# Kernel tuning notes

Hardware: AMD Instinct MI355X
Metric: run time of the kernel (lower is better)

Reference implementation:

```python
import jax, jax.numpy as jnp
import numpy as np

B, N, D = 16384, 20, 13  # batch of states, agents per state, per-agent joint-state dim
SELF_STATE = 6           # self_state_size in SARL


def setup_inputs() -> dict:
    key = jax.random.key(0)
    ks = jax.random.split(key, 16)

    def init(k, fi, fo):
        # haiku MLP default: truncated-normal-ish std 1/sqrt(fan_in), zero bias
        return jax.random.normal(k, (fi, fo), jnp.float32) / np.float32(np.sqrt(fi))

    z = lambda n: jnp.zeros((n,), jnp.float32)
    return {
        "x": jax.random.normal(ks[0], (B, N, D), jnp.float32),
        # mlp1: 13 -> 150 -> 100, relu, activate_final=True
        "w1a": init(ks[1], D, 150), "b1a": z(150),
        "w1b": init(ks[2], 150, 100), "b1b": z(100),
        # attention: 200 -> 100 -> 100 -> 1
        "wa0": init(ks[3], 200, 100), "ba0": z(100),
        "wa1": init(ks[4], 100, 100), "ba1": z(100),
        "wa2": init(ks[5], 100, 1), "ba2": z(1),
        # mlp2: 100 -> 100 -> 50
        "w2a": init(ks[6], 100, 100), "b2a": z(100),
        "w2b": init(ks[7], 100, 50), "b2b": z(50),
        # mlp3: 56 -> 150 -> 100 -> 100 -> 1
        "w3a": init(ks[8], SELF_STATE + 50, 150), "b3a": z(150),
        "w3b": init(ks[9], 150, 100), "b3b": z(100),
        "w3c": init(ks[10], 100, 100), "b3c": z(100),
        "w3d": init(ks[11], 100, 1), "b3d": z(1),
    }


def reference(x, w1a, b1a, w1b, b1b, wa0, ba0, wa1, ba1, wa2, ba2,
              w2a, b2a, w2b, b2b, w3a, b3a, w3b, b3b, w3c, b3c, w3d, b3d):
    relu = jax.nn.relu
    # mlp1 (activate_final=True): [B,N,100]
    h1 = relu(relu(x @ w1a + b1a) @ w1b + b1b)
    # mean-pool over agents -> global state, broadcast + concat: [B,N,200]
    g = jnp.mean(h1, axis=1, keepdims=True)
    att_in = jnp.concatenate([h1, jnp.broadcast_to(g, h1.shape)], axis=-1)
    # attention MLP -> scores [B,N], softmax over agents
    s = relu(att_in @ wa0 + ba0)
    s = relu(s @ wa1 + ba1)
    scores = (s @ wa2 + ba2)[..., 0]
    attn = jax.nn.softmax(scores, axis=-1)
    # mlp2 features [B,N,50], softmax-weighted sum over agents -> [B,50]
    f = relu(h1 @ w2a + b2a) @ w2b + b2b
    wf = jnp.einsum('bnf,bn->bf', f, attn)
    # concat self-state (first row's first 6 dims) with pooled features -> [B,56]
    self_state = x[:, 0, :SELF_STATE]
    m = jnp.concatenate([self_state, wf], axis=-1)
    # mlp3: 56 -> 150 -> 100 -> 100 -> 1
    h = relu(m @ w3a + b3a)
    h = relu(h @ w3b + b3b)
    h = relu(h @ w3c + b3c)
    return h @ w3d + b3d  # [B,1] state value
```

## Files before the change

### kernel.cpp

```cpp
#include <hip/hip_runtime.h>
#include <math.h>

#define NT     512
#define NWAVES 8
#define GB     4
#define NTOK   20
#define NTT_P  5

typedef _Float16 f16x8 __attribute__((ext_vector_type(8)));
typedef _Float16 f16x4 __attribute__((ext_vector_type(4)));
typedef _Float16 f16x2 __attribute__((ext_vector_type(2)));
typedef float    f32x4 __attribute__((ext_vector_type(4)));

#define PHASE_BAR() do {                                      \
    asm volatile("s_waitcnt lgkmcnt(0)" ::: "memory");        \
    __builtin_amdgcn_s_barrier();                             \
    asm volatile("" ::: "memory");                            \
    __builtin_amdgcn_sched_barrier(0);                        \
} while (0)

#define WS_W1A  0
#define WS_W1B  5120
#define WS_WA0  23040
#define WS_WA1  37376
#define WS_W2A  51712
#define WS_W2B  66048
#define WS_W3A  74240
#define WS_W3B  84480
#define WS_W3C  102400
#define WS_WA0H 116736
#define WS_TOTAL 131072
#define WB_BASE 65536
#define WB_B1A  0
#define WB_B1B  160
#define WB_BA0  272
#define WB_BA1  384
#define WB_B2A  496
#define WB_B2B  608
#define WB_B3A  672
#define WB_B3B  832
#define WB_B3C  944
#define WB_WA2  1056
#define WB_N    1168
#define PREP_TOTAL (WS_TOTAL + WB_N)
#define WS_MV   135168

#define LH_A    0
#define LH_B    12160
#define LH_C    23040
#define LH_T1   LH_A
#define LH_S1   LH_A
#define LH_F1   LH_A
#define LH_H1   LH_B
#define LH_FF   LH_B
#define LH_GQ   LH_C
#define LF_PART 11520
#define LF_GB   12672
#define LF_ATT  13120
#define LF_SS   13200
#define LDS_DW  13224
#define LDS_BYTES (LDS_DW * 4)

#define TB      64
#define TL_MV   0
#define TL_HA   4608
#define TL_HB   15360
#define TL_HC   24064
#define LDS_T_DW   16384
#define LDS_T_BYTES (LDS_T_DW * 4)

__device__ __forceinline__ void prep_one(const float* __restrict__ src, _Float16* dst,
                                         int local, int N, int K, int Ks)
{
    int n = local / Ks, k = local - n * Ks;
    dst[local] = (_Float16)((n < N && k < K) ? src[k * N + n] : 0.f);
}
__device__ __forceinline__ void prep_b(const float* __restrict__ src, float* dst,
                                       int idx, int N)
{
    dst[idx] = (idx < N) ? src[idx] : 0.f;
}

__global__ __launch_bounds__(256)
void prep_kernel(const float* __restrict__ w1a, const float* __restrict__ w1b,
                 const float* __restrict__ wa0, const float* __restrict__ wa1,
                 const float* __restrict__ w2a, const float* __restrict__ w2b,
                 const float* __restrict__ w3a, const float* __restrict__ w3b,
                 const float* __restrict__ w3c, const float* __restrict__ wa2,
                 const float* __restrict__ b1a, const float* __restrict__ b1b,
                 const float* __restrict__ ba0, const float* __restrict__ ba1,
                 const float* __restrict__ b2a, const float* __restrict__ b2b,
                 const float* __restrict__ b3a, const float* __restrict__ b3b,
                 const float* __restrict__ b3c,
                 _Float16* __restrict__ ws)
{
    int g = blockIdx.x * 256 + threadIdx.x;
    if (g >= PREP_TOTAL) return;
    if (g >= WS_TOTAL) {
        float* wb = (float*)ws + WB_BASE;
        int l = g - WS_TOTAL;
        if (l < WB_B1B)      prep_b(b1a, wb + WB_B1A, l - WB_B1A, 150);
        else if (l < WB_BA0) prep_b(b1b, wb + WB_B1B, l - WB_B1B, 100);
        else if (l < WB_BA1) prep_b(ba0, wb + WB_BA0, l - WB_BA0, 100);
        else if (l < WB_B2A) prep_b(ba1, wb + WB_BA1, l - WB_BA1, 100);
        else if (l < WB_B2B) prep_b(b2a, wb + WB_B2A, l - WB_B2A, 100);
        else if (l < WB_B3A) prep_b(b2b, wb + WB_B2B, l - WB_B2B, 50);
        else if (l < WB_B3B) prep_b(b3a, wb + WB_B3A, l - WB_B3A, 150);
        else if (l < WB_B3C) prep_b(b3b, wb + WB_B3B, l - WB_B3B, 100);
        else if (l < WB_WA2) prep_b(b3c, wb + WB_B3C, l - WB_B3C, 100);
        else                 prep_b(wa2, wb + WB_WA2, l - WB_WA2, 100);
        return;
    }
    if (g < WS_W1B)       prep_one(w1a, ws + WS_W1A, g - WS_W1A, 150, 13, 32);
    else if (g < WS_WA0)  prep_one(w1b, ws + WS_W1B, g - WS_W1B, 100, 150, 160);
    else if (g < WS_WA1)  prep_one(wa0, ws + WS_WA0, g - WS_WA0, 100, 100, 128);
    else if (g < WS_W2A)  prep_one(wa1, ws + WS_WA1, g - WS_WA1, 100, 100, 128);
    else if (g < WS_W2B)  prep_one(w2a, ws + WS_W2A, g - WS_W2A, 100, 100, 128);
    else if (g < WS_W3A)  prep_one(w2b, ws + WS_W2B, g - WS_W2B,  50, 100, 128);
    else if (g < WS_W3B)  prep_one(w3a, ws + WS_W3A, g - WS_W3A, 150,  56, 64);
    else if (g < WS_W3C)  prep_one(w3b, ws + WS_W3B, g - WS_W3B, 100, 150, 160);
    else if (g < WS_WA0H) prep_one(w3c, ws + WS_W3C, g - WS_W3C, 100, 100, 128);
    else                  prep_one(wa0 + 100 * 100, ws + WS_WA0H, g - WS_WA0H, 100, 100, 128);
}

template<int KT, int MTL, int NW>
struct WC {
    static constexpr int IPW = (MTL + NW - 1) / NW;
    f16x8 wf[IPW][KT];
    f32x4 bv[IPW];
};

template<int KT, int MTL, int NW, bool LOADB>
__device__ __forceinline__ void load_w(WC<KT, MTL, NW>& W,
                                       const _Float16* __restrict__ WT, const int Bs,
                                       const float* __restrict__ biasp,
                                       const int wv, const int lane)
{
    const int cl = lane & 15, kq = lane >> 4;
#pragma unroll
    for (int ii = 0; ii < WC<KT, MTL, NW>::IPW; ++ii) {
        const int mt = wv + ii * NW;
        if (mt < MTL) {
            const _Float16* Wp = WT + (mt * 16 + cl) * Bs + kq * 8;
#pragma unroll
            for (int kt = 0; kt < KT; ++kt) W.wf[ii][kt] = *(const f16x8*)(Wp + kt * 32);
            if (LOADB) W.bv[ii] = *(const f32x4*)(biasp + mt * 16 + kq * 4);
        }
    }
}

template<int KT, int MTL, int NTT, bool RELU, int BMODE, int OMODE, int CLW, int NW>
__device__ __forceinline__ void gemm_c(const WC<KT, MTL, NW>& W,
                                       const _Float16* X, const int Xs,
                                       const float* gbias,
                                       _Float16* Y, const int Ys,
                                       float* part, const float* __restrict__ wa2p,
                                       const int wv, const int lane)
{
    const int cl = lane & 15, kq = lane >> 4;
#pragma unroll
    for (int ii = 0; ii < WC<KT, MTL, NW>::IPW; ++ii) {
        const int mt = wv + ii * NW;
        if (mt >= MTL) break;
        const int fb = mt * 16 + kq * 4;
#pragma unroll
        for (int nt = 0; nt < NTT; ++nt) {
            const _Float16* Xp = X + (nt * 16 + cl) * Xs + kq * 8;
            f16x8 xf[KT];
#pragma unroll
            for (int kt = 0; kt < KT; ++kt) xf[kt] = *(const f16x8*)(Xp + kt * 32);
            f32x4 acc = {0.f, 0.f, 0.f, 0.f};
#pragma unroll
            for (int kt = 0; kt < KT; ++kt)
                acc = __builtin_amdgcn_mfma_f32_16x16x32_f16(W.wf[ii][kt], xf[kt], acc, 0, 0, 0);
            const int token = nt * 16 + cl;
            if (OMODE == 1) {
                if (cl < GB) {
                    f32x4 o = acc + W.bv[ii];
                    *(f32x4*)((float*)Y + cl * 112 + fb) = o;
                }
            } else if (OMODE == 2) {
                f32x4 y = acc + W.bv[ii];
                y[0] = fmaxf(y[0], 0.f); y[1] = fmaxf(y[1], 0.f);
                y[2] = fmaxf(y[2], 0.f); y[3] = fmaxf(y[3], 0.f);
                f32x4 w4 = *(const f32x4*)(wa2p + fb);
                float p = y[0] * w4[0] + y[1] * w4[1] + y[2] * w4[2] + y[3] * w4[3];
                p += __shfl_xor(p, 16);
                p += __shfl_xor(p, 32);
                if (kq == 0) part[token * 8 + mt] = p;
            } else {
                f32x4 bb;
                if (BMODE == 1)
                    bb = *(const f32x4*)(gbias + (token / NTOK) * 112 + fb);
                else
                    bb = W.bv[ii];
                f32x4 y = acc + bb;
                if (RELU) {
                    y[0] = fmaxf(y[0], 0.f); y[1] = fmaxf(y[1], 0.f);
                    y[2] = fmaxf(y[2], 0.f); y[3] = fmaxf(y[3], 0.f);
                }
                if (fb < CLW) {
                    f16x4 o = { (_Float16)y[0], (_Float16)y[1],
                                (_Float16)y[2], (_Float16)y[3] };
                    *(f16x4*)(Y + token * Ys + fb) = o;
                }
            }
        }
    }
}

__global__ __launch_bounds__(NT, 6)
void vnet_kernel(const float* __restrict__ x,
                 const float* __restrict__ ba2,
                 const _Float16* __restrict__ wsh,
                 _Float16* __restrict__ mvg)
{
    extern __shared__ float lds_f[];
    _Float16* lds_h = (_Float16*)lds_f;

    const int tid  = threadIdx.x;
    const int lane = tid & 63, wv = tid >> 6;
    const int b0   = blockIdx.x * GB;
    const float* wb = (const float*)wsh + WB_BASE;

    _Float16* xa  = lds_h + LH_C;
    _Float16* gqh = lds_h + LH_GQ;
    _Float16* h1w = lds_h + LH_H1;
    float* gbias = lds_f + LF_GB;
    float* att   = lds_f + LF_ATT;
    float* ss    = lds_f + LF_SS;
    float* part  = lds_f + LF_PART;

    WC<1, 10, 8> Wp2;
    WC<5, 7, 8>  Wp3;
    WC<4, 7, 8>  Wa, Wb;
    WC<4, 4, 4>  Wm4;

    load_w<1, 10, 8, true>(Wp2, wsh + WS_W1A, 32, wb + WB_B1A, wv, lane);
    const float* xg = x + (size_t)b0 * (NTOK * 13);
    for (int t = tid; t < GB * NTOK * 13; t += NT) {
        int row = t / 13, d = t - row * 13;
        xa[row * 40 + d] = (_Float16)xg[t];
    }
    for (int t = tid; t < 80 * 27; t += NT) {
        int row = t / 27, c = 13 + (t - row * 27);
        xa[row * 40 + c] = (_Float16)0.f;
    }
    for (int t = tid; t < 80 * 24; t += NT) {
        int row = t / 24, c = 112 + (t - row * 24);
        h1w[row * 136 + c] = (_Float16)0.f;
    }
    if (tid < 8) h1w[tid] = (_Float16)0.f;
    if (tid < GB * 6) {
        int b = tid / 6, d = tid - b * 6;
        ss[tid] = xg[b * (NTOK * 13) + d];
    }
    PHASE_BAR();

    load_w<5, 7, 8, true>(Wp3, wsh + WS_W1B, 160, wb + WB_B1B, wv, lane);
    gemm_c<1, 10, NTT_P, true, 0, 0, 152, 8>(Wp2, xa, 40, nullptr,
        lds_h + LH_T1, 152, nullptr, nullptr, wv, lane);
    PHASE_BAR();

    gemm_c<5, 7, NTT_P, true, 0, 0, 10000, 8>(Wp3, lds_h + LH_T1, 152, nullptr,
        h1w, 136, nullptr, nullptr, wv, lane);
    PHASE_BAR();

    load_w<4, 7, 8, true>(Wa, wsh + WS_WA0H, 128, wb + WB_BA0, wv, lane);
    const _Float16* h1 = h1w;
    const uint* h1u = (const uint*)h1;
    for (int t = tid; t < GB * 50; t += NT) {
        int b = t / 50, cp = t - b * 50;
        float s0 = 0.f, s1 = 0.f;
#pragma unroll
        for (int n = 0; n < NTOK; ++n) {
            uint v = h1u[(b * NTOK + n) * 68 + cp];
            f16x2 p = *(const f16x2*)&v;
            s0 += (float)p.x; s1 += (float)p.y;
        }
        f16x2 g = { (_Float16)(s0 * 0.05f), (_Float16)(s1 * 0.05f) };
        *(f16x2*)(gqh + b * 136 + 2 * cp) = g;
    }
    PHASE_BAR();

    load_w<4, 7, 8, false>(Wb, wsh + WS_WA0, 128, nullptr, wv, lane);
    gemm_c<4, 7, 1, false, 0, 1, 10000, 8>(Wa, gqh, 136, nullptr,
        (_Float16*)gbias, 0, nullptr, nullptr, wv, lane);
    PHASE_BAR();

    load_w<4, 7, 8, true>(Wa, wsh + WS_WA1, 128, wb + WB_BA1, wv, lane);
    gemm_c<4, 7, NTT_P, true, 1, 0, 10000, 8>(Wb, h1, 136, gbias,
        lds_h + LH_S1, 136, nullptr, nullptr, wv, lane);
    PHASE_BAR();

    load_w<4, 7, 8, true>(Wb, wsh + WS_W2A, 128, wb + WB_B2A, wv, lane);
    gemm_c<4, 7, NTT_P, true, 0, 2, 10000, 8>(Wa, lds_h + LH_S1, 136, nullptr,
        nullptr, 0, part, wb + WB_WA2, wv, lane);
    PHASE_BAR();

    load_w<4, 4, 4, true>(Wm4, wsh + WS_W2B, 128, wb + WB_B2B, wv, lane);
    gemm_c<4, 7, NTT_P, true, 0, 0, 10000, 8>(Wb, h1, 136, nullptr,
        lds_h + LH_F1, 136, nullptr, nullptr, wv, lane);
    PHASE_BAR();

    if (wv < 4) {
        gemm_c<4, 4, NTT_P, false, 0, 0, 10000, 4>(Wm4, lds_h + LH_F1, 136,
            nullptr, lds_h + LH_FF, 72, nullptr, nullptr, wv, lane);
    } else {
        const int b = wv - 4;
        float sc = -1e30f;
        if (lane < NTOK) {
            sc = ba2[0];
            const float* pr = part + (b * NTOK + lane) * 8;
#pragma unroll
            for (int m = 0; m < 7; ++m) sc += pr[m];
        }
        float mx = sc;
#pragma unroll
        for (int off = 16; off; off >>= 1) mx = fmaxf(mx, __shfl_xor(mx, off, 32));
        float e = (lane < NTOK) ? expf(sc - mx) : 0.f;
        float s = e;
#pragma unroll
        for (int off = 16; off; off >>= 1) s += __shfl_xor(s, off, 32);
        if (lane < NTOK) att[b * NTOK + lane] = e / s;
    }
    PHASE_BAR();

    const _Float16* fh = lds_h + LH_FF;
    for (int t = tid; t < GB * 64; t += NT) {
        int b = t >> 6, c = t & 63;
        float v = 0.f;
        if (c < 6) {
            v = ss[b * 6 + c];
        } else if (c < 56) {
            const int cc = c - 6;
            const float* ab = att + b * NTOK;
            float acc = 0.f;
#pragma unroll
            for (int n = 0; n < NTOK; ++n)
                acc = fmaf((float)fh[(b * NTOK + n) * 72 + cc], ab[n], acc);
            v = acc;
        }
        mvg[(size_t)(b0 + b) * 64 + c] = (_Float16)v;
    }
}

__global__ __launch_bounds__(NT)
void tail_kernel(const _Float16* __restrict__ mvg,
                 const float* __restrict__ w3d, const float* __restrict__ b3d,
                 const _Float16* __restrict__ wsh,
                 float* __restrict__ outp)
{
    extern __shared__ float lds_f[];
    _Float16* lds_h = (_Float16*)lds_f;

    const int tid  = threadIdx.x;
    const int lane = tid & 63, wv = tid >> 6;
    const int g0   = blockIdx.x * TB;
    const float* wb = (const float*)wsh + WB_BASE;

    WC<2, 10, 8> Wt1; WC<5, 7, 8> Wt2; WC<4, 7, 8> Wt3;
    load_w<2, 10, 8, true>(Wt1, wsh + WS_W3A, 64, wb + WB_B3A, wv, lane);

    _Float16* mvT = lds_h + TL_MV;
    {
        const uint* src = (const uint*)(mvg + (size_t)g0 * 64);
        uint* dst = (uint*)mvT;
        for (int t = tid; t < TB * 32; t += NT) {
            int row = t >> 5, c = t & 31;
            dst[row * 36 + c] = src[t];
        }
    }
    for (int t = tid; t < (TL_HC - TL_HB) / 2; t += NT)
        ((uint*)(lds_h + TL_HB))[t] = 0u;
    __syncthreads();

    load_w<5, 7, 8, true>(Wt2, wsh + WS_W3B, 160, wb + WB_B3B, wv, lane);
    gemm_c<2, 10, 4, true, 0, 0, 10000, 8>(Wt1, mvT, 72, nullptr,
        lds_h + TL_HA, 168, nullptr, nullptr, wv, lane);
    __syncthreads();

    load_w<4, 7, 8, true>(Wt3, wsh + WS_W3C, 128, wb + WB_B3C, wv, lane);
    gemm_c<5, 7, 4, true, 0, 0, 10000, 8>(Wt2, lds_h + TL_HA, 168, nullptr,
        lds_h + TL_HB, 136, nullptr, nullptr, wv, lane);
    __syncthreads();

    gemm_c<4, 7, 4, true, 0, 0, 10000, 8>(Wt3, lds_h + TL_HB, 136, nullptr,
        lds_h + TL_HC, 136, nullptr, nullptr, wv, lane);
    __syncthreads();

    {
        const int b = tid >> 3, kl = tid & 7;
        const _Float16* hc = lds_h + TL_HC + b * 136;
        float acc = 0.f;
#pragma unroll 13
        for (int k = kl; k < 100; k += 8)
            acc = fmaf((float)hc[k], w3d[k], acc);
        acc += __shfl_xor(acc, 1);
        acc += __shfl_xor(acc, 2);
        acc += __shfl_xor(acc, 4);
        if (kl == 0) outp[g0 + b] = acc + b3d[0];
    }
}

extern "C" void kernel_launch(void* const* d_in, const int* in_sizes, int n_in,
                              void* d_out, int out_size, void* d_ws, size_t ws_size,
                              hipStream_t stream)
{
    const float* x   = (const float*)d_in[0];
    const float* w1a = (const float*)d_in[1];
    const float* b1a = (const float*)d_in[2];
    const float* w1b = (const float*)d_in[3];
    const float* b1b = (const float*)d_in[4];
    const float* wa0 = (const float*)d_in[5];
    const float* ba0 = (const float*)d_in[6];
    const float* wa1 = (const float*)d_in[7];
    const float* ba1 = (const float*)d_in[8];
    const float* wa2 = (const float*)d_in[9];
    const float* ba2 = (const float*)d_in[10];
    const float* w2a = (const float*)d_in[11];
    const float* b2a = (const float*)d_in[12];
    const float* w2b = (const float*)d_in[13];
    const float* b2b = (const float*)d_in[14];
    const float* w3a = (const float*)d_in[15];
    const float* b3a = (const float*)d_in[16];
    const float* w3b = (const float*)d_in[17];
    const float* b3b = (const float*)d_in[18];
    const float* w3c = (const float*)d_in[19];
    const float* b3c = (const float*)d_in[20];
    const float* w3d = (const float*)d_in[21];
    const float* b3d = (const float*)d_in[22];
    float* outp = (float*)d_out;
    _Float16* wsh = (_Float16*)d_ws;
    _Float16* mvg = wsh + WS_MV;

    hipFuncSetAttribute((const void*)vnet_kernel,
                        hipFuncAttributeMaxDynamicSharedMemorySize, LDS_BYTES);
    hipFuncSetAttribute((const void*)tail_kernel,
                        hipFuncAttributeMaxDynamicSharedMemorySize, LDS_T_BYTES);

    hipLaunchKernelGGL(prep_kernel, dim3((PREP_TOTAL + 255) / 256), dim3(256),
                       0, stream,
                       w1a, w1b, wa0, wa1, w2a, w2b, w3a, w3b, w3c, wa2,
                       b1a, b1b, ba0, ba1, b2a, b2b, b3a, b3b, b3c, wsh);

    const int B = 16384;
    hipLaunchKernelGGL(vnet_kernel, dim3(B / GB), dim3(NT), LDS_BYTES, stream,
                       x, ba2, wsh, mvg);
    hipLaunchKernelGGL(tail_kernel, dim3(B / TB), dim3(NT), LDS_T_BYTES, stream,
                       mvg, w3d, b3d, wsh, outp);
}
```

Measured before the change: 115.9 us.

## Load weights inside each GEMM and pair M-tiles per wave in vnet kernel

```diff
diff --git a/kernel.cpp b/kernel.cpp
--- a/kernel.cpp
+++ b/kernel.cpp
@@ -123,43 +123,32 @@
     else                  prep_one(wa0 + 100 * 100, ws + WS_WA0H, g - WS_WA0H, 100, 100, 128);
 }
 
-template<int KT, int MTL, int NW>
-struct WC {
-    static constexpr int IPW = (MTL + NW - 1) / NW;
+template<int KT, int MTL, int NTT, bool RELU, int BMODE, int OMODE, int CLW, int NW>
+__device__ __forceinline__ void gemm_sw(const _Float16* X, const int Xs,
+                                        const _Float16* __restrict__ WT, const int Bs,
+                                        const float* __restrict__ biasp,
+                                        const float* gbias,
+                                        _Float16* Y, const int Ys,
+                                        float* part, const float* __restrict__ wa2p,
+                                        const int wv, const int lane)
+{
+    const int cl = lane & 15, kq = lane >> 4;
+    constexpr int IPW = (MTL + NW - 1) / NW;
     f16x8 wf[IPW][KT];
     f32x4 bv[IPW];
-};
-
-template<int KT, int MTL, int NW, bool LOADB>
-__device__ __forceinline__ void load_w(WC<KT, MTL, NW>& W,
-                                       const _Float16* __restrict__ WT, const int Bs,
-                                       const float* __restrict__ biasp,
-                                       const int wv, const int lane)
-{
-    const int cl = lane & 15, kq = lane >> 4;
-#pragma unroll
-    for (int ii = 0; ii < WC<KT, MTL, NW>::IPW; ++ii) {
+#pragma unroll
+    for (int ii = 0; ii < IPW; ++ii) {
         const int mt = wv + ii * NW;
         if (mt < MTL) {
             const _Float16* Wp = WT + (mt * 16 + cl) * Bs + kq * 8;
 #pragma unroll
-            for (int kt = 0; kt < KT; ++kt) W.wf[ii][kt] = *(const f16x8*)(Wp + kt * 32);
-            if (LOADB) W.bv[ii] = *(const f32x4*)(biasp + mt * 16 + kq * 4);
-        }
-    }
-}
-
-template<int KT, int MTL, int NTT, bool RELU, int BMODE, int OMODE, int CLW, int NW>
-__device__ __forceinline__ void gemm_c(const WC<KT, MTL, NW>& W,
-                                       const _Float16* X, const int Xs,
-                                       const float* gbias,
-                                       _Float16* Y, const int Ys,
-                                       float* part, const float* __restrict__ wa2p,
-                                       const int wv, const int lane)
-{
-    const int cl = lane & 15, kq = lane >> 4;
-#pragma unroll
-    for (int ii = 0; ii < WC<KT, MTL, NW>::IPW; ++ii) {
+            for (int kt = 0; kt < KT; ++kt) wf[ii][kt] = *(const f16x8*)(Wp + kt * 32);
+            if (BMODE == 0)
+                bv[ii] = *(const f32x4*)(biasp + mt * 16 + kq * 4);
+        }
+    }
+#pragma unroll
+    for (int ii = 0; ii < IPW; ++ii) {
         const int mt = wv + ii * NW;
         if (mt >= MTL) break;
         const int fb = mt * 16 + kq * 4;
@@ -172,15 +161,15 @@
             f32x4 acc = {0.f, 0.f, 0.f, 0.f};
 #pragma unroll
             for (int kt = 0; kt < KT; ++kt)
-                acc = __builtin_amdgcn_mfma_f32_16x16x32_f16(W.wf[ii][kt], xf[kt], acc, 0, 0, 0);
+                acc = __builtin_amdgcn_mfma_f32_16x16x32_f16(wf[ii][kt], xf[kt], acc, 0, 0, 0);
             const int token = nt * 16 + cl;
             if (OMODE == 1) {
                 if (cl < GB) {
-                    f32x4 o = acc + W.bv[ii];
+                    f32x4 o = acc + bv[ii];
                     *(f32x4*)((float*)Y + cl * 112 + fb) = o;
                 }
             } else if (OMODE == 2) {
-                f32x4 y = acc + W.bv[ii];
+                f32x4 y = acc + bv[ii];
                 y[0] = fmaxf(y[0], 0.f); y[1] = fmaxf(y[1], 0.f);
                 y[2] = fmaxf(y[2], 0.f); y[3] = fmaxf(y[3], 0.f);
                 f32x4 w4 = *(const f32x4*)(wa2p + fb);
@@ -193,7 +182,7 @@
                 if (BMODE == 1)
                     bb = *(const f32x4*)(gbias + (token / NTOK) * 112 + fb);
                 else
-                    bb = W.bv[ii];
+                    bb = bv[ii];
                 f32x4 y = acc + bb;
                 if (RELU) {
                     y[0] = fmaxf(y[0], 0.f); y[1] = fmaxf(y[1], 0.f);
@@ -209,6 +198,85 @@
     }
 }
 
+template<bool RELU, int BMODE, int OMODE>
+__device__ __forceinline__ void pair_epi(f32x4 acc, f32x4 bvv, int mt, int token,
+                                         int kq, const float* gbias,
+                                         _Float16* Y, int Ys, float* part,
+                                         const float* __restrict__ wa2p)
+{
+    const int fb = mt * 16 + kq * 4;
+    if (OMODE == 2) {
+        f32x4 y = acc + bvv;
+        y[0] = fmaxf(y[0], 0.f); y[1] = fmaxf(y[1], 0.f);
+        y[2] = fmaxf(y[2], 0.f); y[3] = fmaxf(y[3], 0.f);
+        f32x4 w4 = *(const f32x4*)(wa2p + fb);
+        float p = y[0] * w4[0] + y[1] * w4[1] + y[2] * w4[2] + y[3] * w4[3];
+        p += __shfl_xor(p, 16);
+        p += __shfl_xor(p, 32);
+        if (kq == 0) part[token * 8 + mt] = p;
+    } else {
+        f32x4 bb = (BMODE == 1)
+            ? *(const f32x4*)(gbias + (token / NTOK) * 112 + fb) : bvv;
+        f32x4 y = acc + bb;
+        if (RELU) {
+            y[0] = fmaxf(y[0], 0.f); y[1] = fmaxf(y[1], 0.f);
+            y[2] = fmaxf(y[2], 0.f); y[3] = fmaxf(y[3], 0.f);
+        }
+        f16x4 o = { (_Float16)y[0], (_Float16)y[1],
+                    (_Float16)y[2], (_Float16)y[3] };
+        *(f16x4*)(Y + token * Ys + fb) = o;
+    }
+}
+
+template<int KT, int MTL, bool RELU, int BMODE, int OMODE>
+__device__ __forceinline__ void gemm_pair(const _Float16* X, const int Xs,
+                                          const _Float16* __restrict__ WT, const int Bs,
+                                          const float* __restrict__ biasp,
+                                          const float* gbias,
+                                          _Float16* Y, const int Ys,
+                                          float* part, const float* __restrict__ wa2p,
+                                          const int wv, const int lane)
+{
+    const int cl = lane & 15, kq = lane >> 4;
+    const int p = wv >> 1, h = wv & 1;
+    const int mt0 = 2 * p, mt1 = 2 * p + 1;
+    const bool two = (mt1 < MTL);
+    f16x8 w0[KT], w1[KT];
+    f32x4 b0 = {0.f, 0.f, 0.f, 0.f}, b1 = {0.f, 0.f, 0.f, 0.f};
+    {
+        const _Float16* Wp0 = WT + (mt0 * 16 + cl) * Bs + kq * 8;
+#pragma unroll
+        for (int kt = 0; kt < KT; ++kt) w0[kt] = *(const f16x8*)(Wp0 + kt * 32);
+        if (BMODE == 0) b0 = *(const f32x4*)(biasp + mt0 * 16 + kq * 4);
+        if (two) {
+            const _Float16* Wp1 = WT + (mt1 * 16 + cl) * Bs + kq * 8;
+#pragma unroll
+            for (int kt = 0; kt < KT; ++kt) w1[kt] = *(const f16x8*)(Wp1 + kt * 32);
+            if (BMODE == 0) b1 = *(const f32x4*)(biasp + mt1 * 16 + kq * 4);
+        }
+    }
+#pragma unroll
+    for (int i = 0; i < 3; ++i) {
+        if (h && i == 2) break;
+        const int nt = h ? (3 + i) : i;
+        const _Float16* Xp = X + (nt * 16 + cl) * Xs + kq * 8;
+        f16x8 xf[KT];
+#pragma unroll
+        for (int kt = 0; kt < KT; ++kt) xf[kt] = *(const f16x8*)(Xp + kt * 32);
+        f32x4 a0 = {0.f, 0.f, 0.f, 0.f}, a1 = {0.f, 0.f, 0.f, 0.f};
+#pragma unroll
+        for (int kt = 0; kt < KT; ++kt) {
+            a0 = __builtin_amdgcn_mfma_f32_16x16x32_f16(w0[kt], xf[kt], a0, 0, 0, 0);
+            if (two)
+                a1 = __builtin_amdgcn_mfma_f32_16x16x32_f16(w1[kt], xf[kt], a1, 0, 0, 0);
+        }
+        const int token = nt * 16 + cl;
+        pair_epi<RELU, BMODE, OMODE>(a0, b0, mt0, token, kq, gbias, Y, Ys, part, wa2p);
+        if (two)
+            pair_epi<RELU, BMODE, OMODE>(a1, b1, mt1, token, kq, gbias, Y, Ys, part, wa2p);
+    }
+}
+
 __global__ __launch_bounds__(NT, 6)
 void vnet_kernel(const float* __restrict__ x,
                  const float* __restrict__ ba2,
@@ -231,12 +299,6 @@
     float* ss    = lds_f + LF_SS;
     float* part  = lds_f + LF_PART;
 
-    WC<1, 10, 8> Wp2;
-    WC<5, 7, 8>  Wp3;
-    WC<4, 7, 8>  Wa, Wb;
-    WC<4, 4, 4>  Wm4;
-
-    load_w<1, 10, 8, true>(Wp2, wsh + WS_W1A, 32, wb + WB_B1A, wv, lane);
     const float* xg = x + (size_t)b0 * (NTOK * 13);
     for (int t = tid; t < GB * NTOK * 13; t += NT) {
         int row = t / 13, d = t - row * 13;
@@ -257,16 +319,14 @@
     }
     PHASE_BAR();
 
-    load_w<5, 7, 8, true>(Wp3, wsh + WS_W1B, 160, wb + WB_B1B, wv, lane);
-    gemm_c<1, 10, NTT_P, true, 0, 0, 152, 8>(Wp2, xa, 40, nullptr,
-        lds_h + LH_T1, 152, nullptr, nullptr, wv, lane);
-    PHASE_BAR();
-
-    gemm_c<5, 7, NTT_P, true, 0, 0, 10000, 8>(Wp3, lds_h + LH_T1, 152, nullptr,
-        h1w, 136, nullptr, nullptr, wv, lane);
-    PHASE_BAR();
-
-    load_w<4, 7, 8, true>(Wa, wsh + WS_WA0H, 128, wb + WB_BA0, wv, lane);
+    gemm_sw<1, 10, NTT_P, true, 0, 0, 152, 8>(xa, 40, wsh + WS_W1A, 32,
+        wb + WB_B1A, nullptr, lds_h + LH_T1, 152, nullptr, nullptr, wv, lane);
+    PHASE_BAR();
+
+    gemm_sw<5, 7, NTT_P, true, 0, 0, 10000, 8>(lds_h + LH_T1, 152, wsh + WS_W1B,
+        160, wb + WB_B1B, nullptr, h1w, 136, nullptr, nullptr, wv, lane);
+    PHASE_BAR();
+
     const _Float16* h1 = h1w;
     const uint* h1u = (const uint*)h1;
     for (int t = tid; t < GB * 50; t += NT) {
@@ -275,37 +335,34 @@
 #pragma unroll
         for (int n = 0; n < NTOK; ++n) {
             uint v = h1u[(b * NTOK + n) * 68 + cp];
-            f16x2 p = *(const f16x2*)&v;
-            s0 += (float)p.x; s1 += (float)p.y;
+            f16x2 pq = *(const f16x2*)&v;
+            s0 += (float)pq.x; s1 += (float)pq.y;
         }
         f16x2 g = { (_Float16)(s0 * 0.05f), (_Float16)(s1 * 0.05f) };
         *(f16x2*)(gqh + b * 136 + 2 * cp) = g;
     }
     PHASE_BAR();
 
-    load_w<4, 7, 8, false>(Wb, wsh + WS_WA0, 128, nullptr, wv, lane);
-    gemm_c<4, 7, 1, false, 0, 1, 10000, 8>(Wa, gqh, 136, nullptr,
-        (_Float16*)gbias, 0, nullptr, nullptr, wv, lane);
-    PHASE_BAR();
-
-    load_w<4, 7, 8, true>(Wa, wsh + WS_WA1, 128, wb + WB_BA1, wv, lane);
-    gemm_c<4, 7, NTT_P, true, 1, 0, 10000, 8>(Wb, h1, 136, gbias,
+    gemm_sw<4, 7, 1, false, 0, 1, 10000, 8>(gqh, 136, wsh + WS_WA0H, 128,
+        wb + WB_BA0, nullptr, (_Float16*)gbias, 0, nullptr, nullptr, wv, lane);
+    PHASE_BAR();
+
+    gemm_pair<4, 7, true, 1, 0>(h1, 136, wsh + WS_WA0, 128, nullptr, gbias,
         lds_h + LH_S1, 136, nullptr, nullptr, wv, lane);
     PHASE_BAR();
 
-    load_w<4, 7, 8, true>(Wb, wsh + WS_W2A, 128, wb + WB_B2A, wv, lane);
-    gemm_c<4, 7, NTT_P, true, 0, 2, 10000, 8>(Wa, lds_h + LH_S1, 136, nullptr,
-        nullptr, 0, part, wb + WB_WA2, wv, lane);
-    PHASE_BAR();
-
-    load_w<4, 4, 4, true>(Wm4, wsh + WS_W2B, 128, wb + WB_B2B, wv, lane);
-    gemm_c<4, 7, NTT_P, true, 0, 0, 10000, 8>(Wb, h1, 136, nullptr,
-        lds_h + LH_F1, 136, nullptr, nullptr, wv, lane);
+    gemm_pair<4, 7, true, 0, 2>(lds_h + LH_S1, 136, wsh + WS_WA1, 128,
+        wb + WB_BA1, nullptr, nullptr, 0, part, wb + WB_WA2, wv, lane);
+    PHASE_BAR();
+
+    gemm_pair<4, 7, true, 0, 0>(h1, 136, wsh + WS_W2A, 128, wb + WB_B2A,
+        nullptr, lds_h + LH_F1, 136, nullptr, nullptr, wv, lane);
     PHASE_BAR();
 
     if (wv < 4) {
-        gemm_c<4, 4, NTT_P, false, 0, 0, 10000, 4>(Wm4, lds_h + LH_F1, 136,
-            nullptr, lds_h + LH_FF, 72, nullptr, nullptr, wv, lane);
+        gemm_sw<4, 4, NTT_P, false, 0, 0, 10000, 4>(lds_h + LH_F1, 136,
+            wsh + WS_W2B, 128, wb + WB_B2B, nullptr, lds_h + LH_FF, 72,
+            nullptr, nullptr, wv, lane);
     } else {
         const int b = wv - 4;
         float sc = -1e30f;
@@ -345,6 +402,67 @@
     }
 }
 
+template<int KT, int MTL, int NW>
+struct WC {
+    static constexpr int IPW = (MTL + NW - 1) / NW;
+    f16x8 wf[IPW][KT];
+    f32x4 bv[IPW];
+};
+
+template<int KT, int MTL, int NW, bool LOADB>
+__device__ __forceinline__ void load_w(WC<KT, MTL, NW>& W,
+                                       const _Float16* __restrict__ WT, const int Bs,
+                                       const float* __restrict__ biasp,
+                                       const int wv, const int lane)
+{
+    const int cl = lane & 15, kq = lane >> 4;
+#pragma unroll
+    for (int ii = 0; ii < WC<KT, MTL, NW>::IPW; ++ii) {
+        const int mt = wv + ii * NW;
+        if (mt < MTL) {
+            const _Float16* Wp = WT + (mt * 16 + cl) * Bs + kq * 8;
+#pragma unroll
+            for (int kt = 0; kt < KT; ++kt) W.wf[ii][kt] = *(const f16x8*)(Wp + kt * 32);
+            if (LOADB) W.bv[ii] = *(const f32x4*)(biasp + mt * 16 + kq * 4);
+        }
+    }
+}
+
+template<int KT, int MTL, int NTT, bool RELU, int NW>
+__device__ __forceinline__ void gemm_wc(const WC<KT, MTL, NW>& W,
+                                        const _Float16* X, const int Xs,
+                                        _Float16* Y, const int Ys,
+                                        const int wv, const int lane)
+{
+    const int cl = lane & 15, kq = lane >> 4;
+#pragma unroll
+    for (int ii = 0; ii < WC<KT, MTL, NW>::IPW; ++ii) {
+        const int mt = wv + ii * NW;
+        if (mt >= MTL) break;
+        const int fb = mt * 16 + kq * 4;
+#pragma unroll
+        for (int nt = 0; nt < NTT; ++nt) {
+            const _Float16* Xp = X + (nt * 16 + cl) * Xs + kq * 8;
+            f16x8 xf[KT];
+#pragma unroll
+            for (int kt = 0; kt < KT; ++kt) xf[kt] = *(const f16x8*)(Xp + kt * 32);
+            f32x4 acc = {0.f, 0.f, 0.f, 0.f};
+#pragma unroll
+            for (int kt = 0; kt < KT; ++kt)
+                acc = __builtin_amdgcn_mfma_f32_16x16x32_f16(W.wf[ii][kt], xf[kt], acc, 0, 0, 0);
+            const int token = nt * 16 + cl;
+            f32x4 y = acc + W.bv[ii];
+            if (RELU) {
+                y[0] = fmaxf(y[0], 0.f); y[1] = fmaxf(y[1], 0.f);
+                y[2] = fmaxf(y[2], 0.f); y[3] = fmaxf(y[3], 0.f);
+            }
+            f16x4 o = { (_Float16)y[0], (_Float16)y[1],
+                        (_Float16)y[2], (_Float16)y[3] };
+            *(f16x4*)(Y + token * Ys + fb) = o;
+        }
+    }
+}
+
 __global__ __launch_bounds__(NT)
 void tail_kernel(const _Float16* __restrict__ mvg,
                  const float* __restrict__ w3d, const float* __restrict__ b3d,
@@ -376,17 +494,14 @@
     __syncthreads();
 
     load_w<5, 7, 8, true>(Wt2, wsh + WS_W3B, 160, wb + WB_B3B, wv, lane);
-    gemm_c<2, 10, 4, true, 0, 0, 10000, 8>(Wt1, mvT, 72, nullptr,
-        lds_h + TL_HA, 168, nullptr, nullptr, wv, lane);
+    gemm_wc<2, 10, 4, true, 8>(Wt1, mvT, 72, lds_h + TL_HA, 168, wv, lane);
     __syncthreads();
 
     load_w<4, 7, 8, true>(Wt3, wsh + WS_W3C, 128, wb + WB_B3C, wv, lane);
-    gemm_c<5, 7, 4, true, 0, 0, 10000, 8>(Wt2, lds_h + TL_HA, 168, nullptr,
-        lds_h + TL_HB, 136, nullptr, nullptr, wv, lane);
+    gemm_wc<5, 7, 4, true, 8>(Wt2, lds_h + TL_HA, 168, lds_h + TL_HB, 136, wv, lane);
     __syncthreads();
 
-    gemm_c<4, 7, 4, true, 0, 0, 10000, 8>(Wt3, lds_h + TL_HB, 136, nullptr,
-        lds_h + TL_HC, 136, nullptr, nullptr, wv, lane);
+    gemm_wc<4, 7, 4, true, 8>(Wt3, lds_h + TL_HB, 136, lds_h + TL_HC, 136, wv, lane);
     __syncthreads();
 
     {
```

Result: slower. 197.4 us (+70.4%).
